# Kernel tuning notes

Measured on AMD Instinct MI355X. Metric: run time of the kernel, lower is better.

The kernel has to match this reference:

```python
import jax, jax.numpy as jnp
import numpy as np

N, D_IN, D_C, D_Q, K = 4096, 64, 32, 128, 3


def setup_inputs() -> dict:
    key = jax.random.key(0)
    ks = jax.random.split(key, 16)
    rn = lambda k, shp, s: jax.random.normal(k, shp, dtype=jnp.float32) * s
    inp = {
        "x": rn(ks[0], (N, D_IN), 1.0),
        "comms": rn(ks[1], (N, D_C), 0.1),
        # dense positive transition matrix (all entries nonzero -> the
        # trans==0 -> -inf masking step is a faithful no-op here)
        "trans": jax.random.uniform(ks[2], (N, N), dtype=jnp.float32, minval=0.01, maxval=1.0),
        "mask": jnp.ones((N,), dtype=jnp.int32),
        # encoding: Linear(num_inputs + comm_channels, ch_q)
        "W_enc": rn(ks[3], (D_IN + D_C, D_Q), 1.0 / np.sqrt(D_IN + D_C)),
        "b_enc": rn(ks[4], (D_Q,), 0.01),
        # att_decoding[k]: Linear(ch_q, ch_q)
        "W_ad": rn(ks[5], (K, D_Q, D_Q), 1.0 / np.sqrt(D_Q)),
        "b_ad": rn(ks[6], (K, D_Q), 0.01),
        # att[k]: Linear(2*ch_q, 1)
        "w_att": rn(ks[7], (K, 2 * D_Q), 1.0 / np.sqrt(2 * D_Q)),
        "b_att": rn(ks[8], (K,), 0.01),
        # att_vectors[k]: Linear(ch_q, ch_q)
        "W_av": rn(ks[9], (K, D_Q, D_Q), 1.0 / np.sqrt(D_Q)),
        "b_av": rn(ks[10], (K, D_Q), 0.01),
        # decoding: Linear(ch_q, 1)
        "W_dec": rn(ks[11], (D_Q,), 1.0 / np.sqrt(D_Q)),
        "b_dec": rn(ks[12], (), 0.01),
    }
    return inp


def reference(x, comms, trans, mask, W_enc, b_enc, W_ad, b_ad, w_att, b_att,
              W_av, b_av, W_dec, b_dec):
    dq = W_ad.shape[-1]
    # encoding of [node features, communication vector]
    h = jnp.concatenate([x, comms], axis=-1) @ W_enc + b_enc          # (n, dq)
    # trans.transpose(0,1); zeros -> -inf (additive log-mask)
    tb = trans.T
    tb = jnp.where(tb == 0, -jnp.inf, tb)                              # (n, n)
    for k in range(K):
        att = h @ W_ad[k] + b_ad[k]                                    # (n, dq)
        # concat-GAT score: score[i,j] = w_a . att[j] + w_b . att[i] + b
        # (decomposition of Linear(cat(att_t, att_t^T)) -> avoids n x n x 2dq)
        wa, wb = w_att[k, :dq], w_att[k, dq:]
        score = (att @ wb)[:, None] + (att @ wa)[None, :] + b_att[k]   # (n, n)
        focus = jax.nn.softmax(score + tb, axis=1)                     # (n, n)
        v = h @ W_av[k] + b_av[k]                                      # (n, dq)
        h = focus @ v                                                  # (n, dq)
    out = h @ W_dec + b_dec                                            # (n,)
    # final masking (args.rl = False branch): masked nodes -> -inf
    s = out + jnp.where(mask == 0, -jnp.inf, 0.0).astype(out.dtype)
    return s
```

## Files before the change

kernel.cpp:

```cpp
#include <hip/hip_runtime.h>
#include <math.h>

#define N 4096
#define DQ 128
#define DIN 64
#define DC 32
#define NT 9
#define PSTRIDE 144
#define NIT (N / 16)

typedef __attribute__((ext_vector_type(8))) short short8;
typedef __attribute__((ext_vector_type(8))) _Float16 half8;
typedef __attribute__((ext_vector_type(4))) float f32x4;

__device__ __forceinline__ unsigned short f2h(float x) {
  return __builtin_bit_cast(unsigned short, (_Float16)x);
}

__device__ __forceinline__ void v_phase(const float* hs_row, float p,
    const float* __restrict__ W_av_k, const float* __restrict__ b_av_k,
    int r, int d4, unsigned short* shh, unsigned short* shl) {
  float a[4] = {b_av_k[d4], b_av_k[d4 + 1], b_av_k[d4 + 2], b_av_k[d4 + 3]};
  for (int c = 0; c < DQ; ++c) {
    const float hv = hs_row[c];
    const float4 w = *(const float4*)&W_av_k[c * DQ + d4];
    a[0] += hv * w.x; a[1] += hv * w.y; a[2] += hv * w.z; a[3] += hv * w.w;
  }
  const int nt = d4 >> 4;
#pragma unroll
  for (int e = 0; e < 4; ++e) {
    const float val = p * a[e];
    const _Float16 hi = (_Float16)val;
    const _Float16 lo = (_Float16)(val - (float)hi);
    const int ix = nt * 128 + ((d4 + e) & 15) * 8 + r;
    shh[ix] = __builtin_bit_cast(unsigned short, hi);
    shl[ix] = __builtin_bit_cast(unsigned short, lo);
  }
  const int c32 = d4 >> 2;
  if (c32 < 16) {
    const int ix = 8 * 128 + c32 * 8 + r;
    if (c32 == 0) {
      const _Float16 phi = (_Float16)p;
      const _Float16 plo = (_Float16)(p - (float)phi);
      shh[ix] = __builtin_bit_cast(unsigned short, phi);
      shl[ix] = __builtin_bit_cast(unsigned short, plo);
    } else {
      shh[ix] = 0; shl[ix] = 0;
    }
  }
}

__device__ __forceinline__ void v_store(int tid, int blk,
    const unsigned short* shh, const unsigned short* shl,
    unsigned short* __restrict__ Vhi, unsigned short* __restrict__ Vlo) {
  const int kt = blk >> 2, quad = blk & 3;
  if (tid < NT * 16) {
    const int nt = tid >> 4, l15 = tid & 15;
    const size_t dst = (((size_t)kt * NT + nt) * 64 + quad * 16 + l15) * 8;
    *(short8*)(Vhi + dst) = *(const short8*)&shh[nt * 128 + l15 * 8];
    *(short8*)(Vlo + dst) = *(const short8*)&shl[nt * 128 + l15 * 8];
  }
}

__global__ __launch_bounds__(256) void kVS0(const float* __restrict__ x,
    const float* __restrict__ comms, const float* __restrict__ W_enc,
    const float* __restrict__ b_enc, const float* __restrict__ W_ad_k,
    const float* __restrict__ wa, const float* __restrict__ W_av_k,
    const float* __restrict__ b_av_k,
    unsigned short* __restrict__ Vhi, unsigned short* __restrict__ Vlo) {
  __shared__ float xs[8][96];
  __shared__ float hs[8][DQ];
  __shared__ float u[DQ];
  __shared__ float pb[8];
  __shared__ __align__(16) unsigned short shh[NT * 128];
  __shared__ __align__(16) unsigned short shl[NT * 128];
  const int tid = threadIdx.x;
  const int blk = blockIdx.x;
  if (tid < 128) {
    const float4 v = *(const float4*)&x[(size_t)blk * 8 * DIN + tid * 4];
    const int idx = tid * 4, r = idx >> 6, c = idx & 63;
    xs[r][c] = v.x; xs[r][c + 1] = v.y; xs[r][c + 2] = v.z; xs[r][c + 3] = v.w;
  } else if (tid < 192) {
    const int t = tid - 128;
    const float4 v = *(const float4*)&comms[(size_t)blk * 8 * DC + t * 4];
    const int idx = t * 4, r = idx >> 5, c = idx & 31;
    xs[r][64 + c] = v.x; xs[r][64 + c + 1] = v.y; xs[r][64 + c + 2] = v.z; xs[r][64 + c + 3] = v.w;
  }
  if (tid < DQ) {
    float s = 0.f;
    const float* wrow = &W_ad_k[tid * DQ];
    for (int q = 0; q < DQ; ++q) s += wrow[q] * wa[q];
    u[tid] = s;
  }
  __syncthreads();
  const int r = tid >> 5;
  const int c32 = tid & 31;
  const int d4 = c32 * 4;
  {
    float a0 = b_enc[d4], a1 = b_enc[d4 + 1], a2 = b_enc[d4 + 2], a3 = b_enc[d4 + 3];
    for (int c = 0; c < 96; ++c) {
      const float hv = xs[r][c];
      const float4 w = *(const float4*)&W_enc[c * DQ + d4];
      a0 += hv * w.x; a1 += hv * w.y; a2 += hv * w.z; a3 += hv * w.w;
    }
    hs[r][d4] = a0; hs[r][d4 + 1] = a1; hs[r][d4 + 2] = a2; hs[r][d4 + 3] = a3;
  }
  __syncthreads();
  float part = 0.f;
  for (int c = c32; c < DQ; c += 32) part += hs[r][c] * u[c];
#pragma unroll
  for (int m = 16; m > 0; m >>= 1) part += __shfl_xor(part, m, 32);
  if (c32 == 0) pb[r] = __expf(part);
  __syncthreads();
  v_phase(hs[r], pb[r], W_av_k, b_av_k, r, d4, shh, shl);
  __syncthreads();
  v_store(tid, blk, shh, shl, Vhi, Vlo);
}

__global__ __launch_bounds__(256) void kVSR(const float* __restrict__ P,
    const float* __restrict__ W_ad_k, const float* __restrict__ wa,
    const float* __restrict__ W_av_k, const float* __restrict__ b_av_k,
    unsigned short* __restrict__ Vhi, unsigned short* __restrict__ Vlo,
    int ksplit) {
  __shared__ float hs[8][DQ];
  __shared__ float u[DQ];
  __shared__ float pb[8];
  __shared__ __align__(16) unsigned short shh[NT * 128];
  __shared__ __align__(16) unsigned short shl[NT * 128];
  const int tid = threadIdx.x;
  const int r = tid >> 5;
  const int c32 = tid & 31;
  const int d4 = c32 * 4;
  const int j = blockIdx.x * 8 + r;
  if (tid < DQ) {
    float s = 0.f;
    const float* wrow = &W_ad_k[tid * DQ];
    for (int q = 0; q < DQ; ++q) s += wrow[q] * wa[q];
    u[tid] = s;
  }
  float4 num = {0.f, 0.f, 0.f, 0.f};
  float den = 0.f;
  for (int s = 0; s < ksplit; ++s) {
    const float* b = &P[((size_t)s * N + j) * PSTRIDE];
    const float4 v = *(const float4*)&b[d4];
    num.x += v.x; num.y += v.y; num.z += v.z; num.w += v.w;
    den += b[128];
  }
  const float inv = 1.f / den;
  hs[r][d4] = num.x * inv; hs[r][d4 + 1] = num.y * inv;
  hs[r][d4 + 2] = num.z * inv; hs[r][d4 + 3] = num.w * inv;
  __syncthreads();
  float part = 0.f;
  for (int c = c32; c < DQ; c += 32) part += hs[r][c] * u[c];
#pragma unroll
  for (int m = 16; m > 0; m >>= 1) part += __shfl_xor(part, m, 32);
  if (c32 == 0) pb[r] = __expf(part);
  __syncthreads();
  v_phase(hs[r], pb[r], W_av_k, b_av_k, r, d4, shh, shl);
  __syncthreads();
  v_store(tid, blockIdx.x, shh, shl, Vhi, Vlo);
}

template <bool PRE>
__global__ __launch_bounds__(64, PRE ? 2 : 1) void kGemmM(
    const float* __restrict__ trans, unsigned short* __restrict__ Ef,
    const unsigned short* __restrict__ Vhi, const unsigned short* __restrict__ Vlo,
    float* __restrict__ P, int kchunk) {
  const int lane = threadIdx.x;
  const int quad = lane >> 4, l15 = lane & 15;
  const int it0 = blockIdx.x * 2;
  const int i0 = it0 * 16;
  const int k0 = blockIdx.y * kchunk;
  const int nsteps = kchunk >> 5;
  const size_t kt0 = (size_t)(k0 >> 5);

  f32x4 acc[2][NT];
#pragma unroll
  for (int ti = 0; ti < 2; ++ti)
#pragma unroll
    for (int nt = 0; nt < NT; ++nt) acc[ti][nt] = (f32x4){0.f, 0.f, 0.f, 0.f};

  half8 Bh[NT], Bl[NT], Ah[2];
  float araw[2][8];

  if (PRE) {
#pragma unroll
    for (int nt = 0; nt < NT; ++nt) {
      const size_t bix = ((kt0 * NT + nt) * 64 + lane) * 8;
      Bh[nt] = __builtin_bit_cast(half8, *(const short8*)(Vhi + bix));
      Bl[nt] = __builtin_bit_cast(half8, *(const short8*)(Vlo + bix));
    }
#pragma unroll
    for (int ti = 0; ti < 2; ++ti) {
      const size_t aix = ((kt0 * NIT + it0 + ti) * 64 + lane) * 8;
      Ah[ti] = __builtin_bit_cast(half8, *(const short8*)(Ef + aix));
    }
  } else {
#pragma unroll
    for (int ti = 0; ti < 2; ++ti) {
      const float* aptr = trans + (size_t)(k0 + quad * 8) * N + i0 + ti * 16 + l15;
#pragma unroll
      for (int jj = 0; jj < 8; ++jj) araw[ti][jj] = aptr[(size_t)jj * N];
    }
  }

  for (int t = 0; t < nsteps; ++t) {
    const size_t kt = kt0 + t;
    const bool more = (t + 1 < nsteps);
    half8 nBh[NT], nBl[NT], nAh[2];
    float nar[2][8];
    if (PRE) {
      if (more) {
#pragma unroll
        for (int ti = 0; ti < 2; ++ti) {
          const size_t aix = (((kt + 1) * NIT + it0 + ti) * 64 + lane) * 8;
          nAh[ti] = __builtin_bit_cast(half8, *(const short8*)(Ef + aix));
        }
#pragma unroll
        for (int nt = 0; nt < NT; ++nt) {
          const size_t bix = (((kt + 1) * NT + nt) * 64 + lane) * 8;
          nBh[nt] = __builtin_bit_cast(half8, *(const short8*)(Vhi + bix));
          nBl[nt] = __builtin_bit_cast(half8, *(const short8*)(Vlo + bix));
        }
      }
    } else {
#pragma unroll
      for (int nt = 0; nt < NT; ++nt) {
        const size_t bix = ((kt * NT + nt) * 64 + lane) * 8;
        Bh[nt] = __builtin_bit_cast(half8, *(const short8*)(Vhi + bix));
        Bl[nt] = __builtin_bit_cast(half8, *(const short8*)(Vlo + bix));
      }
      if (more) {
#pragma unroll
        for (int ti = 0; ti < 2; ++ti) {
          const float* ap2 = trans + (size_t)(k0 + (t + 1) * 32 + quad * 8) * N + i0 + ti * 16 + l15;
#pragma unroll
          for (int jj = 0; jj < 8; ++jj) nar[ti][jj] = ap2[(size_t)jj * N];
        }
      }
#pragma unroll
      for (int ti = 0; ti < 2; ++ti) {
        unsigned short hb[8];
#pragma unroll
        for (int jj = 0; jj < 8; ++jj) hb[jj] = f2h(__expf(araw[ti][jj]));
        const short8 s = {(short)hb[0], (short)hb[1], (short)hb[2], (short)hb[3],
                          (short)hb[4], (short)hb[5], (short)hb[6], (short)hb[7]};
        Ah[ti] = __builtin_bit_cast(half8, s);
        *(short8*)(Ef + ((kt * NIT + it0 + ti) * 64 + lane) * 8) = s;
      }
    }
#pragma unroll
    for (int nt = 0; nt < NT; ++nt) {
#pragma unroll
      for (int ti = 0; ti < 2; ++ti) {
        acc[ti][nt] = __builtin_amdgcn_mfma_f32_16x16x32_f16(Ah[ti], Bh[nt], acc[ti][nt], 0, 0, 0);
        acc[ti][nt] = __builtin_amdgcn_mfma_f32_16x16x32_f16(Ah[ti], Bl[nt], acc[ti][nt], 0, 0, 0);
      }
    }
    if (more) {
      if (PRE) {
        Ah[0] = nAh[0]; Ah[1] = nAh[1];
#pragma unroll
        for (int nt = 0; nt < NT; ++nt) { Bh[nt] = nBh[nt]; Bl[nt] = nBl[nt]; }
      } else {
#pragma unroll
        for (int ti = 0; ti < 2; ++ti)
#pragma unroll
          for (int jj = 0; jj < 8; ++jj) araw[ti][jj] = nar[ti][jj];
      }
    }
  }
  float* Pb = P + (size_t)blockIdx.y * N * PSTRIDE;
#pragma unroll
  for (int ti = 0; ti < 2; ++ti) {
#pragma unroll
    for (int nt = 0; nt < NT; ++nt) {
#pragma unroll
      for (int r = 0; r < 4; ++r) {
        const int i = i0 + ti * 16 + quad * 4 + r;
        Pb[(size_t)i * PSTRIDE + nt * 16 + l15] = acc[ti][nt][r];
      }
    }
  }
}

__global__ __launch_bounds__(256) void kOutR(const float* __restrict__ P,
    const float* __restrict__ W_dec, const float* __restrict__ b_dec,
    const int* __restrict__ mask, float* __restrict__ out, int ksplit) {
  __shared__ float red[256];
  const int tid = threadIdx.x;
  const int d = tid & 127;
  const int i = blockIdx.x * 2 + (tid >> 7);
  float num = 0.f, den = 0.f;
  for (int s = 0; s < ksplit; ++s) {
    const float* b = &P[((size_t)s * N + i) * PSTRIDE];
    num += b[d];
    den += b[128];
  }
  red[tid] = num * W_dec[d];
  __syncthreads();
  for (int st = 64; st > 0; st >>= 1) {
    if (d < st) red[tid] += red[tid + st];
    __syncthreads();
  }
  if (d == 0) out[i] = (mask[i] == 0) ? -INFINITY : red[tid] / den + b_dec[0];
}

extern "C" void kernel_launch(void* const* d_in, const int* in_sizes, int n_in,
                              void* d_out, int out_size, void* d_ws, size_t ws_size,
                              hipStream_t stream) {
  (void)in_sizes; (void)n_in; (void)out_size;
  const float* x     = (const float*)d_in[0];
  const float* comms = (const float*)d_in[1];
  const float* trans = (const float*)d_in[2];
  const int*   mask  = (const int*)d_in[3];
  const float* W_enc = (const float*)d_in[4];
  const float* b_enc = (const float*)d_in[5];
  const float* W_ad  = (const float*)d_in[6];
  const float* w_att = (const float*)d_in[8];
  const float* W_av  = (const float*)d_in[10];
  const float* b_av  = (const float*)d_in[11];
  const float* W_dec = (const float*)d_in[12];
  const float* b_dec = (const float*)d_in[13];
  float* out         = (float*)d_out;

  char* ws = (char*)d_ws;
  unsigned short* Vhi = (unsigned short*)ws;  ws += (size_t)N * PSTRIDE * 2;
  unsigned short* Vlo = (unsigned short*)ws;  ws += (size_t)N * PSTRIDE * 2;
  unsigned short* Ef  = (unsigned short*)ws;  ws += (size_t)N * N * 2;
  float* P = (float*)ws;
  const size_t fixedB = (size_t)N * PSTRIDE * 4 + (size_t)N * N * 2;
  const size_t perB   = (size_t)N * PSTRIDE * 4;
  const int ksplit = (ws_size >= fixedB + 16 * perB) ? 16 : 8;
  const int kchunk = N / ksplit;

  for (int k = 0; k < 3; ++k) {
    const float* W_ad_k = W_ad + (size_t)k * DQ * DQ;
    const float* wa     = w_att + (size_t)k * 2 * DQ;
    const float* W_av_k = W_av + (size_t)k * DQ * DQ;
    const float* b_av_k = b_av + (size_t)k * DQ;
    if (k == 0) {
      kVS0<<<N / 8, 256, 0, stream>>>(x, comms, W_enc, b_enc, W_ad_k, wa,
                                      W_av_k, b_av_k, Vhi, Vlo);
      kGemmM<false><<<dim3(N / 32, ksplit), 64, 0, stream>>>(
          trans, Ef, Vhi, Vlo, P, kchunk);
    } else {
      kVSR<<<N / 8, 256, 0, stream>>>(P, W_ad_k, wa, W_av_k, b_av_k,
                                      Vhi, Vlo, ksplit);
      kGemmM<true><<<dim3(N / 32, ksplit), 64, 0, stream>>>(
          trans, Ef, Vhi, Vlo, P, kchunk);
    }
  }
  kOutR<<<N / 2, 256, 0, stream>>>(P, W_dec, b_dec, mask, out, ksplit);
}
```

Baseline: 257.8 us.

## Split exp of trans into a separate kernel and share B tiles across waves via LDS

Result: faster. 245.9 us (-4.6%).

```diff
diff --git a/kernel.cpp b/kernel.cpp
--- a/kernel.cpp
+++ b/kernel.cpp
@@ -7,7 +7,8 @@
 #define DC 32
 #define NT 9
 #define PSTRIDE 144
-#define NIT (N / 16)
+#define NIT 256
+#define LDSF (NT * 512)
 
 typedef __attribute__((ext_vector_type(8))) short short8;
 typedef __attribute__((ext_vector_type(8))) _Float16 half8;
@@ -15,6 +16,38 @@
 
 __device__ __forceinline__ unsigned short f2h(float x) {
   return __builtin_bit_cast(unsigned short, (_Float16)x);
+}
+__device__ __forceinline__ void async16(unsigned short* lds, const unsigned short* g) {
+  __builtin_amdgcn_global_load_lds(
+      (const __attribute__((address_space(1))) void*)g,
+      (__attribute__((address_space(3))) void*)lds, 16, 0, 0);
+}
+
+__global__ __launch_bounds__(256) void kExp(const float* __restrict__ trans,
+                                            unsigned short* __restrict__ Ef) {
+  __shared__ float sh[32 * 65];
+  const int tid = threadIdx.x;
+  const int ig = blockIdx.x;
+  const int kt = blockIdx.y;
+  const int r = tid >> 3;
+  const int c8 = (tid & 7) * 8;
+  const float* src = &trans[((size_t)kt * 32 + r) * N + ig * 64 + c8];
+  const float4 v0 = *(const float4*)src;
+  const float4 v1 = *(const float4*)(src + 4);
+  float* d = &sh[r * 65 + c8];
+  d[0] = __expf(v0.x); d[1] = __expf(v0.y); d[2] = __expf(v0.z); d[3] = __expf(v0.w);
+  d[4] = __expf(v1.x); d[5] = __expf(v1.y); d[6] = __expf(v1.z); d[7] = __expf(v1.w);
+  __syncthreads();
+  const int itl = tid >> 6;
+  const int lane = tid & 63;
+  const int quad = lane >> 4, l15 = lane & 15;
+  const int col = itl * 16 + l15;
+  unsigned short hb[8];
+#pragma unroll
+  for (int jj = 0; jj < 8; ++jj) hb[jj] = f2h(sh[(quad * 8 + jj) * 65 + col]);
+  const short8 s = {(short)hb[0], (short)hb[1], (short)hb[2], (short)hb[3],
+                    (short)hb[4], (short)hb[5], (short)hb[6], (short)hb[7]};
+  *(short8*)(Ef + (((size_t)kt * NIT + ig * 4 + itl) * 64 + lane) * 8) = s;
 }
 
 __device__ __forceinline__ void v_phase(const float* hs_row, float p,
@@ -161,123 +194,76 @@
   v_store(tid, blockIdx.x, shh, shl, Vhi, Vlo);
 }
 
-template <bool PRE>
-__global__ __launch_bounds__(64, PRE ? 2 : 1) void kGemmM(
-    const float* __restrict__ trans, unsigned short* __restrict__ Ef,
+__global__ __launch_bounds__(256) void kGemm(
+    const unsigned short* __restrict__ Ef,
     const unsigned short* __restrict__ Vhi, const unsigned short* __restrict__ Vlo,
-    float* __restrict__ P, int kchunk) {
-  const int lane = threadIdx.x;
+    float* __restrict__ P, int nsteps) {
+  __shared__ __align__(16) unsigned short ldsB[2][2 * LDSF];
+  const int tid = threadIdx.x;
+  const int w = tid >> 6, lane = tid & 63;
   const int quad = lane >> 4, l15 = lane & 15;
-  const int it0 = blockIdx.x * 2;
-  const int i0 = it0 * 16;
-  const int k0 = blockIdx.y * kchunk;
-  const int nsteps = kchunk >> 5;
-  const size_t kt0 = (size_t)(k0 >> 5);
-
+  const int it0 = blockIdx.x * 8 + w * 2;
+  const size_t kt0 = (size_t)blockIdx.y * nsteps;
+
+#pragma unroll
+  for (int c = w; c < 2 * NT; c += 4) {
+    const unsigned short* g = (c < NT)
+        ? Vhi + (kt0 * NT + c) * 512 + lane * 8
+        : Vlo + (kt0 * NT + (c - NT)) * 512 + lane * 8;
+    async16(&ldsB[0][c * 512], g);
+  }
+  half8 Ah[2];
+#pragma unroll
+  for (int ti = 0; ti < 2; ++ti)
+    Ah[ti] = __builtin_bit_cast(half8,
+        *(const short8*)(Ef + ((kt0 * NIT + it0 + ti) * 64 + lane) * 8));
   f32x4 acc[2][NT];
 #pragma unroll
   for (int ti = 0; ti < 2; ++ti)
 #pragma unroll
     for (int nt = 0; nt < NT; ++nt) acc[ti][nt] = (f32x4){0.f, 0.f, 0.f, 0.f};
-
-  half8 Bh[NT], Bl[NT], Ah[2];
-  float araw[2][8];
-
-  if (PRE) {
+  __syncthreads();
+
+  for (int t = 0; t < nsteps; ++t) {
+    const bool more = (t + 1 < nsteps);
+    half8 nAh[2];
+    if (more) {
+      const size_t ktn = kt0 + t + 1;
+#pragma unroll
+      for (int c = w; c < 2 * NT; c += 4) {
+        const unsigned short* g = (c < NT)
+            ? Vhi + (ktn * NT + c) * 512 + lane * 8
+            : Vlo + (ktn * NT + (c - NT)) * 512 + lane * 8;
+        async16(&ldsB[(t + 1) & 1][c * 512], g);
+      }
+#pragma unroll
+      for (int ti = 0; ti < 2; ++ti)
+        nAh[ti] = __builtin_bit_cast(half8,
+            *(const short8*)(Ef + ((ktn * NIT + it0 + ti) * 64 + lane) * 8));
+    }
+    const unsigned short* bb = ldsB[t & 1];
 #pragma unroll
     for (int nt = 0; nt < NT; ++nt) {
-      const size_t bix = ((kt0 * NT + nt) * 64 + lane) * 8;
-      Bh[nt] = __builtin_bit_cast(half8, *(const short8*)(Vhi + bix));
-      Bl[nt] = __builtin_bit_cast(half8, *(const short8*)(Vlo + bix));
-    }
-#pragma unroll
-    for (int ti = 0; ti < 2; ++ti) {
-      const size_t aix = ((kt0 * NIT + it0 + ti) * 64 + lane) * 8;
-      Ah[ti] = __builtin_bit_cast(half8, *(const short8*)(Ef + aix));
-    }
-  } else {
-#pragma unroll
-    for (int ti = 0; ti < 2; ++ti) {
-      const float* aptr = trans + (size_t)(k0 + quad * 8) * N + i0 + ti * 16 + l15;
-#pragma unroll
-      for (int jj = 0; jj < 8; ++jj) araw[ti][jj] = aptr[(size_t)jj * N];
-    }
-  }
-
-  for (int t = 0; t < nsteps; ++t) {
-    const size_t kt = kt0 + t;
-    const bool more = (t + 1 < nsteps);
-    half8 nBh[NT], nBl[NT], nAh[2];
-    float nar[2][8];
-    if (PRE) {
-      if (more) {
-#pragma unroll
-        for (int ti = 0; ti < 2; ++ti) {
-          const size_t aix = (((kt + 1) * NIT + it0 + ti) * 64 + lane) * 8;
-          nAh[ti] = __builtin_bit_cast(half8, *(const short8*)(Ef + aix));
-        }
-#pragma unroll
-        for (int nt = 0; nt < NT; ++nt) {
-          const size_t bix = (((kt + 1) * NT + nt) * 64 + lane) * 8;
-          nBh[nt] = __builtin_bit_cast(half8, *(const short8*)(Vhi + bix));
-          nBl[nt] = __builtin_bit_cast(half8, *(const short8*)(Vlo + bix));
-        }
-      }
-    } else {
-#pragma unroll
-      for (int nt = 0; nt < NT; ++nt) {
-        const size_t bix = ((kt * NT + nt) * 64 + lane) * 8;
-        Bh[nt] = __builtin_bit_cast(half8, *(const short8*)(Vhi + bix));
-        Bl[nt] = __builtin_bit_cast(half8, *(const short8*)(Vlo + bix));
-      }
-      if (more) {
-#pragma unroll
-        for (int ti = 0; ti < 2; ++ti) {
-          const float* ap2 = trans + (size_t)(k0 + (t + 1) * 32 + quad * 8) * N + i0 + ti * 16 + l15;
-#pragma unroll
-          for (int jj = 0; jj < 8; ++jj) nar[ti][jj] = ap2[(size_t)jj * N];
-        }
-      }
-#pragma unroll
-      for (int ti = 0; ti < 2; ++ti) {
-        unsigned short hb[8];
-#pragma unroll
-        for (int jj = 0; jj < 8; ++jj) hb[jj] = f2h(__expf(araw[ti][jj]));
-        const short8 s = {(short)hb[0], (short)hb[1], (short)hb[2], (short)hb[3],
-                          (short)hb[4], (short)hb[5], (short)hb[6], (short)hb[7]};
-        Ah[ti] = __builtin_bit_cast(half8, s);
-        *(short8*)(Ef + ((kt * NIT + it0 + ti) * 64 + lane) * 8) = s;
-      }
-    }
+      const half8 Bh = __builtin_bit_cast(half8, *(const short8*)(bb + nt * 512 + lane * 8));
+      const half8 Bl = __builtin_bit_cast(half8, *(const short8*)(bb + LDSF + nt * 512 + lane * 8));
+      acc[0][nt] = __builtin_amdgcn_mfma_f32_16x16x32_f16(Ah[0], Bh, acc[0][nt], 0, 0, 0);
+      acc[0][nt] = __builtin_amdgcn_mfma_f32_16x16x32_f16(Ah[0], Bl, acc[0][nt], 0, 0, 0);
+      acc[1][nt] = __builtin_amdgcn_mfma_f32_16x16x32_f16(Ah[1], Bh, acc[1][nt], 0, 0, 0);
+      acc[1][nt] = __builtin_amdgcn_mfma_f32_16x16x32_f16(Ah[1], Bl, acc[1][nt], 0, 0, 0);
+    }
+    if (more) {
+      Ah[0] = nAh[0]; Ah[1] = nAh[1];
+      __syncthreads();
+    }
+  }
+  float* Pb = P + (size_t)blockIdx.y * N * PSTRIDE;
+#pragma unroll
+  for (int ti = 0; ti < 2; ++ti) {
 #pragma unroll
     for (int nt = 0; nt < NT; ++nt) {
 #pragma unroll
-      for (int ti = 0; ti < 2; ++ti) {
-        acc[ti][nt] = __builtin_amdgcn_mfma_f32_16x16x32_f16(Ah[ti], Bh[nt], acc[ti][nt], 0, 0, 0);
-        acc[ti][nt] = __builtin_amdgcn_mfma_f32_16x16x32_f16(Ah[ti], Bl[nt], acc[ti][nt], 0, 0, 0);
-      }
-    }
-    if (more) {
-      if (PRE) {
-        Ah[0] = nAh[0]; Ah[1] = nAh[1];
-#pragma unroll
-        for (int nt = 0; nt < NT; ++nt) { Bh[nt] = nBh[nt]; Bl[nt] = nBl[nt]; }
-      } else {
-#pragma unroll
-        for (int ti = 0; ti < 2; ++ti)
-#pragma unroll
-          for (int jj = 0; jj < 8; ++jj) araw[ti][jj] = nar[ti][jj];
-      }
-    }
-  }
-  float* Pb = P + (size_t)blockIdx.y * N * PSTRIDE;
-#pragma unroll
-  for (int ti = 0; ti < 2; ++ti) {
-#pragma unroll
-    for (int nt = 0; nt < NT; ++nt) {
-#pragma unroll
       for (int r = 0; r < 4; ++r) {
-        const int i = i0 + ti * 16 + quad * 4 + r;
+        const int i = (it0 + ti) * 16 + quad * 4 + r;
         Pb[(size_t)i * PSTRIDE + nt * 16 + l15] = acc[ti][nt][r];
       }
     }
@@ -332,8 +318,9 @@
   const size_t fixedB = (size_t)N * PSTRIDE * 4 + (size_t)N * N * 2;
   const size_t perB   = (size_t)N * PSTRIDE * 4;
   const int ksplit = (ws_size >= fixedB + 16 * perB) ? 16 : 8;
-  const int kchunk = N / ksplit;
-
+  const int nsteps = (N / ksplit) >> 5;
+
+  kExp<<<dim3(64, 128), 256, 0, stream>>>(trans, Ef);
   for (int k = 0; k < 3; ++k) {
     const float* W_ad_k = W_ad + (size_t)k * DQ * DQ;
     const float* wa     = w_att + (size_t)k * 2 * DQ;
@@ -342,14 +329,11 @@
     if (k == 0) {
       kVS0<<<N / 8, 256, 0, stream>>>(x, comms, W_enc, b_enc, W_ad_k, wa,
                                       W_av_k, b_av_k, Vhi, Vlo);
-      kGemmM<false><<<dim3(N / 32, ksplit), 64, 0, stream>>>(
-          trans, Ef, Vhi, Vlo, P, kchunk);
     } else {
       kVSR<<<N / 8, 256, 0, stream>>>(P, W_ad_k, wa, W_av_k, b_av_k,
                                       Vhi, Vlo, ksplit);
-      kGemmM<true><<<dim3(N / 32, ksplit), 64, 0, stream>>>(
-          trans, Ef, Vhi, Vlo, P, kchunk);
-    }
+    }
+    kGemm<<<dim3(NIT / 8, ksplit), 256, 0, stream>>>(Ef, Vhi, Vlo, P, nsteps);
   }
   kOutR<<<N / 2, 256, 0, stream>>>(P, W_dec, b_dec, mask, out, ksplit);
 }
```
